# Optimization experiments

Measured on AMD Instinct MI355X. Metric: run time of the kernel, lower is better.

Reference implementation:

```python
import jax, jax.numpy as jnp
import numpy as np
from jax import lax

BS = 8  # block size
NF = 64  # num_feat

def _dct_mat(n=BS):
    k = np.arange(n)
    D = np.cos(np.pi * (2 * k[None, :] + 1) * k[:, None] / (2 * n)) * np.sqrt(2.0 / n)
    D[0] = np.sqrt(1.0 / n)
    return jnp.asarray(D, dtype=jnp.float32)  # orthonormal DCT-II basis [8,8]

D_DCT = _dct_mat()

def conv2d(x, w, b, stride=1, padding=0, dilation=1, groups=1):
    out = lax.conv_general_dilated(
        x, w, window_strides=(stride, stride),
        padding=[(padding, padding), (padding, padding)],
        rhs_dilation=(dilation, dilation),
        feature_group_count=groups,
        dimension_numbers=('NCHW', 'OIHW', 'NCHW'))
    return out + b[None, :, None, None]

def block_dct_idct(x, bs=BS):
    # fused per-8x8-block DDCT followed by IDDCT (orthonormal basis ->
    # mathematically identity, computed explicitly as in the original loop)
    B, C, H, W = x.shape
    xb = x.reshape(B, C, H // bs, bs, W // bs, bs)
    CB = jnp.einsum('ij,bchjwk,lk->bchiwl', D_DCT, xb, D_DCT)   # D X D^T
    out = jnp.einsum('ji,bchjwk,kl->bchiwl', D_DCT, CB, D_DCT)  # D^T Y D
    return out.reshape(B, C, H, W)

def setup_inputs() -> dict:
    key = jax.random.key(0)
    ks = jax.random.split(key, 16)
    s = 0.05
    inp = {
        'x': jax.random.normal(ks[0], (2, 72, 256, 256), dtype=jnp.float32),
        'conv_w': jax.random.normal(ks[1], (64, 72, 3, 3), dtype=jnp.float32) * s,
        'conv_b': jnp.zeros((64,), dtype=jnp.float32),
        # 7 distinct directional_dct_layer instances (branch 6 reuses layer 4's weights, as in the source)
        'ddct_w': jax.random.normal(ks[2], (7, 64, 64, 3, 3), dtype=jnp.float32) * s,
        'ddct_b': jnp.zeros((7, 64), dtype=jnp.float32),
        'dctc_w': jax.random.normal(ks[3], (7, 64, 1, 3, 3), dtype=jnp.float32) * s,  # groups=64 depthwise
        'dctc_b': jnp.zeros((7, 64), dtype=jnp.float32),
        'dw1_w': jax.random.normal(ks[4], (32, 72, 3, 3), dtype=jnp.float32) * s,
        'dw1_b': jnp.zeros((32,), dtype=jnp.float32),
        'dw3_w': jax.random.normal(ks[5], (512, 32, 1, 1), dtype=jnp.float32) * s,
        'dw3_b': jnp.zeros((512,), dtype=jnp.float32),
        'ar_w': jax.random.normal(ks[6], (72, 512, 3, 3), dtype=jnp.float32) * s,
        'ar_b': jnp.zeros((72,), dtype=jnp.float32),
    }
    return inp

def reference(x, conv_w, conv_b, ddct_w, ddct_b, dctc_w, dctc_b,
              dw1_w, dw1_b, dw3_w, dw3_b, ar_w, ar_b):
    B, _, H, W = x.shape
    feat = jax.nn.gelu(conv2d(x, conv_w, conv_b, padding=1), approximate=False)
    # branches use layers [0,1,3,4,5,6(->4),7,8]; branch 6 reuses conv_dct_4
    layer_idx = [0, 1, 2, 3, 4, 3, 5, 6]
    outs = []
    for li in layer_idx:
        y = jax.nn.gelu(conv2d(feat, ddct_w[li], ddct_b[li], padding=1), approximate=False) + feat
        y = conv2d(y, dctc_w[li], dctc_b[li], stride=8, padding=2, dilation=2, groups=NF)
        y = block_dct_idct(y)
        y = jax.image.resize(y, (B, NF, H, W), method='bilinear')  # align_corners=False
        outs.append(y)
    w = jax.nn.sigmoid(conv2d(jax.nn.relu(conv2d(x, dw1_w, dw1_b, padding=1)), dw3_w, dw3_b, padding=0))
    gated = jnp.concatenate([o * w[:, i * NF:(i + 1) * NF] for i, o in enumerate(outs)], axis=1)
    return conv2d(gated, ar_w, ar_b, padding=1)
```

## Files before the change

### kernel.cpp

```cpp
#include <hip/hip_runtime.h>
#include <hip/hip_bf16.h>

#define BB 2
#define HH 256
#define WW 256
#define HW (HH*WW)
#define GP 258
#define GPP (GP*GP)

typedef __attribute__((ext_vector_type(8))) short bf16x8;
typedef __attribute__((ext_vector_type(4))) float f32x4;

__device__ __forceinline__ float geluf(float x) {
    return 0.5f * x * (1.0f + erff(x * 0.7071067811865475f));
}

__device__ __forceinline__ ushort f2bf(float f) {
    __hip_bfloat16 h = __float2bfloat16(f);
    return *reinterpret_cast<ushort*>(&h);
}
__device__ __forceinline__ float bf2f(ushort u) {
    uint v = ((uint)u) << 16;
    return *reinterpret_cast<float*>(&v);
}

__device__ __forceinline__ int dec96(int i) {
    int q = i / 3, r = i - q * 3;
    return q * 8 + (r == 0 ? 0 : (r == 1 ? 2 : 6));
}

__global__ __launch_bounds__(256) void xpose_kernel(
    const float* __restrict__ x, ushort* __restrict__ xt)
{
    const int pix = blockIdx.x * 256 + threadIdx.x;
    const int b   = pix >> 16;
    const int rem = pix & 65535;

    uint w[48];
    const float* xb = x + (size_t)b * 72 * HW + rem;
    #pragma unroll
    for (int i = 0; i < 36; ++i) {
        const ushort lo = f2bf(xb[(size_t)(2 * i)     * HW]);
        const ushort hi = f2bf(xb[(size_t)(2 * i + 1) * HW]);
        w[i] = (uint)lo | ((uint)hi << 16);
    }
    #pragma unroll
    for (int i = 36; i < 48; ++i) w[i] = 0;

    uint* dst = reinterpret_cast<uint*>(xt + (size_t)pix * 96);
    #pragma unroll
    for (int k = 0; k < 12; ++k) {
        uint4 u = { w[4*k], w[4*k+1], w[4*k+2], w[4*k+3] };
        *reinterpret_cast<uint4*>(dst + 4 * k) = u;
    }
}

__global__ __launch_bounds__(256) void prepack_w1_kernel(
    const float* __restrict__ conv_w, const float* __restrict__ dw1_w,
    ushort* __restrict__ wpc1)
{
    const int idx = blockIdx.x * 256 + threadIdx.x;
    if (idx >= 9 * 3 * 6 * 64) return;
    const int lane = idx & 63;
    int rest = idx >> 6;
    const int mf = rest % 6; rest /= 6;
    const int cb = rest % 3;
    const int t  = rest / 3;
    const int co  = mf * 16 + (lane & 15);
    const int ci0 = cb * 32 + (lane >> 4) * 8;
    ushort* dst = wpc1 + (size_t)idx * 8;
    #pragma unroll
    for (int j = 0; j < 8; ++j) {
        const int ci = ci0 + j;
        float w = 0.0f;
        if (ci < 72)
            w = (co < 64) ? conv_w[((size_t)co * 72 + ci) * 9 + t]
                          : dw1_w[((size_t)(co - 64) * 72 + ci) * 9 + t];
        dst[j] = f2bf(w);
    }
}

__global__ __launch_bounds__(256) void conv1dw1_mfma_kernel(
    const ushort* __restrict__ xt, const ushort* __restrict__ wpc1,
    const float* __restrict__ conv_b, const float* __restrict__ dw1_b,
    ushort* __restrict__ fg, float* __restrict__ relu1)
{
    const int lane = threadIdx.x & 63;
    const int wave = threadIdx.x >> 6;
    const int l15  = lane & 15;
    const int lg   = lane >> 4;

    const int bid  = blockIdx.x;
    const int b    = bid >> 9;
    const int rest = bid & 511;
    const int y    = rest >> 1;
    const int x0   = (rest & 1) * 128 + wave * 32;

    f32x4 acc[6][2];
    #pragma unroll
    for (int mf = 0; mf < 6; ++mf)
        #pragma unroll
        for (int nf = 0; nf < 2; ++nf)
            acc[mf][nf] = (f32x4){0.f, 0.f, 0.f, 0.f};

    const bf16x8 zero8 = {};

    #pragma unroll 1
    for (int t = 0; t < 9; ++t) {
        const int dy = t / 3 - 1, dx = t % 3 - 1;
        const int yy = y + dy;
        if ((unsigned)yy >= (unsigned)HH) continue;

        const int xA = x0 + l15 + dx;
        const int xB = xA + 16;
        const bool va = (unsigned)xA < (unsigned)WW;
        const bool vb = (unsigned)xB < (unsigned)WW;
        const int xAc = min(max(xA, 0), WW - 1);
        const int xBc = min(xB, WW - 1);

        const ushort* rowbase = xt + ((size_t)(b * HH + yy) * WW) * 96;
        const ushort* pA = rowbase + (size_t)xAc * 96 + lg * 8;
        const ushort* pB = rowbase + (size_t)xBc * 96 + lg * 8;
        const ushort* wp = wpc1 + (size_t)(t * 3) * (6 * 512) + lane * 8;

        #pragma unroll
        for (int cb = 0; cb < 3; ++cb) {
            bf16x8 B0 = *reinterpret_cast<const bf16x8*>(pA + cb * 32);
            bf16x8 B1 = *reinterpret_cast<const bf16x8*>(pB + cb * 32);
            B0 = va ? B0 : zero8;
            B1 = vb ? B1 : zero8;
            const ushort* wpc = wp + (size_t)cb * (6 * 512);
            #pragma unroll
            for (int mf = 0; mf < 6; ++mf) {
                const bf16x8 A = *reinterpret_cast<const bf16x8*>(wpc + mf * 512);
                acc[mf][0] = __builtin_amdgcn_mfma_f32_16x16x32_bf16(A, B0, acc[mf][0], 0, 0, 0);
                acc[mf][1] = __builtin_amdgcn_mfma_f32_16x16x32_bf16(A, B1, acc[mf][1], 0, 0, 0);
            }
        }
    }

    #pragma unroll
    for (int nf = 0; nf < 2; ++nf) {
        const int xx = x0 + nf * 16 + l15;
        ushort* fgp = fg + ((size_t)(b * HH + y) * WW + xx) * 64;
        #pragma unroll
        for (int mf = 0; mf < 4; ++mf) {
            const int co = mf * 16 + lg * 4;
            ushort pk[4];
            #pragma unroll
            for (int r = 0; r < 4; ++r)
                pk[r] = f2bf(geluf(acc[mf][nf][r] + conv_b[co + r]));
            *reinterpret_cast<uint2*>(fgp + co) = *reinterpret_cast<uint2*>(pk);
        }
    }
    #pragma unroll
    for (int mf = 4; mf < 6; ++mf) {
        const int co = (mf - 4) * 16 + lg * 4;
        #pragma unroll
        for (int nf = 0; nf < 2; ++nf) {
            const int xx = x0 + nf * 16 + l15;
            float* op = relu1 + ((size_t)(b * 32 + co) * HH + y) * WW + xx;
            #pragma unroll
            for (int r = 0; r < 4; ++r)
                op[(size_t)r * HW] = fmaxf(acc[mf][nf][r] + dw1_b[co + r], 0.0f);
        }
    }
}

__global__ __launch_bounds__(256) void prepack_wb_kernel(
    const float* __restrict__ ddct_w, ushort* __restrict__ wpb)
{
    const int idx = blockIdx.x * 256 + threadIdx.x;
    if (idx >= 7 * 9 * 2 * 4 * 64) return;
    const int lane = idx & 63;
    int rest = idx >> 6;
    const int mf = rest & 3; rest >>= 2;
    const int cb = rest & 1; rest >>= 1;
    const int t  = rest % 9;
    const int li = rest / 9;
    const int co  = mf * 16 + (lane & 15);
    const int ci0 = cb * 32 + (lane >> 4) * 8;
    ushort* dst = wpb + (size_t)idx * 8;
    #pragma unroll
    for (int j = 0; j < 8; ++j)
        dst[j] = f2bf(ddct_w[(((size_t)li * 64 + co) * 64 + ci0 + j) * 9 + t]);
}

__global__ __launch_bounds__(256) void branch_mfma_kernel(
    const ushort* __restrict__ fg, const ushort* __restrict__ wpb,
    const float* __restrict__ ddct_b, float* __restrict__ ycomp)
{
    const int lane = threadIdx.x & 63;
    const int wave = threadIdx.x >> 6;
    const int l15  = lane & 15;
    const int lg   = lane >> 4;

    int bid = blockIdx.x;
    const int t72 = bid % 72; bid /= 72;
    const int b  = bid & 1;
    const int li = bid >> 1;
    const int widx = t72 * 4 + wave;
    const int r  = widx / 3;
    const int c0 = (widx - r * 3) * 32;
    const int R  = dec96(r);

    const int cA = c0 + l15, cB = cA + 16;
    const int CA = dec96(cA), CB2 = dec96(cB);

    f32x4 acc[4][2];
    #pragma unroll
    for (int mf = 0; mf < 4; ++mf)
        #pragma unroll
        for (int nf = 0; nf < 2; ++nf)
            acc[mf][nf] = (f32x4){0.f, 0.f, 0.f, 0.f};

    const bf16x8 zero8 = {};
    const ushort* fgb = fg + (size_t)b * HW * 64;

    #pragma unroll 1
    for (int t = 0; t < 9; ++t) {
        const int dy = t / 3 - 1, dx = t % 3 - 1;
        const int yy = R + dy;
        if ((unsigned)yy >= (unsigned)HH) continue;

        const int xA = CA + dx, xB = CB2 + dx;
        const bool va = (unsigned)xA < (unsigned)WW;
        const bool vb = (unsigned)xB < (unsigned)WW;
        const int xAc = min(max(xA, 0), WW - 1);
        const int xBc = min(max(xB, 0), WW - 1);

        const ushort* rowb = fgb + (size_t)yy * WW * 64;
        const ushort* pA = rowb + (size_t)xAc * 64 + lg * 8;
        const ushort* pB = rowb + (size_t)xBc * 64 + lg * 8;
        const ushort* wp = wpb + (size_t)((li * 9 + t) * 2) * (4 * 512) + lane * 8;

        #pragma unroll
        for (int cb = 0; cb < 2; ++cb) {
            bf16x8 B0 = *reinterpret_cast<const bf16x8*>(pA + cb * 32);
            bf16x8 B1 = *reinterpret_cast<const bf16x8*>(pB + cb * 32);
            B0 = va ? B0 : zero8;
            B1 = vb ? B1 : zero8;
            const ushort* wpc = wp + (size_t)cb * (4 * 512);
            #pragma unroll
            for (int mf = 0; mf < 4; ++mf) {
                const bf16x8 A = *reinterpret_cast<const bf16x8*>(wpc + mf * 512);
                acc[mf][0] = __builtin_amdgcn_mfma_f32_16x16x32_bf16(A, B0, acc[mf][0], 0, 0, 0);
                acc[mf][1] = __builtin_amdgcn_mfma_f32_16x16x32_bf16(A, B1, acc[mf][1], 0, 0, 0);
            }
        }
    }

    #pragma unroll
    for (int nf = 0; nf < 2; ++nf) {
        const int c = c0 + nf * 16 + l15;
        const int C = dec96(c);
        const ushort* res = fgb + ((size_t)R * WW + C) * 64;
        #pragma unroll
        for (int mf = 0; mf < 4; ++mf) {
            const int co = mf * 16 + lg * 4;
            ushort r4[4];
            *reinterpret_cast<uint2*>(r4) = *reinterpret_cast<const uint2*>(res + co);
            #pragma unroll
            for (int rr = 0; rr < 4; ++rr) {
                const float v = geluf(acc[mf][nf][rr] + ddct_b[li * 64 + co + rr]) + bf2f(r4[rr]);
                ycomp[((((size_t)li * BB + b) * 64 + co + rr) * 96 + r) * 96 + c] = v;
            }
        }
    }
}

__global__ __launch_bounds__(256) void dctc_kernel(
    const float* __restrict__ ycomp, const float* __restrict__ dctc_w,
    const float* __restrict__ dctc_b, float* __restrict__ s_all)
{
    const int idx = blockIdx.x * 256 + threadIdx.x;
    if (idx >= 7 * BB * 64 * 32 * 32) return;
    const int ow = idx & 31;
    const int oh = (idx >> 5) & 31;
    const int c  = (idx >> 10) & 63;
    const int b  = (idx >> 16) & (BB - 1);
    const int li = idx >> 17;

    const float* yc = ycomp + (((size_t)li * BB + b) * 64 + c) * (96 * 96);
    const float* w  = dctc_w + (li * 64 + c) * 9;
    float acc = dctc_b[li * 64 + c];
    #pragma unroll
    for (int ky = 0; ky < 3; ++ky) {
        const int cr = 3 * oh + ky - 1;
        if (cr < 0) continue;
        #pragma unroll
        for (int kx = 0; kx < 3; ++kx) {
            const int cc = 3 * ow + kx - 1;
            if (cc < 0) continue;
            acc = fmaf(yc[cr * 96 + cc], w[ky * 3 + kx], acc);
        }
    }
    s_all[idx] = acc;
}

__global__ __launch_bounds__(256) void prepack_w3_kernel(
    const float* __restrict__ dw3_w, float* __restrict__ dw3t)
{
    const int idx = blockIdx.x * 256 + threadIdx.x;
    if (idx >= 32 * 512) return;
    const int ch = idx & 511;
    const int k  = idx >> 9;
    dw3t[k * 512 + ch] = dw3_w[ch * 32 + k];
}

__global__ __launch_bounds__(256) void halo_zero_kernel(ushort* __restrict__ gt)
{
    const int PB = 2 * GP * 64 + 2 * 256 * 64;
    const int i = blockIdx.x * 256 + threadIdx.x;
    if (i >= BB * PB) return;
    const int b = i / PB;
    int r = i - b * PB;
    size_t px;
    int c4;
    if (r < 2 * GP * 64) {
        const int rr = r / (GP * 64);
        int rem = r - rr * (GP * 64);
        const int xp = rem / 64; c4 = rem % 64;
        px = (size_t)(rr ? GP - 1 : 0) * GP + xp;
    } else {
        r -= 2 * GP * 64;
        const int side = r / (256 * 64);
        int rem = r - side * (256 * 64);
        const int yp = 1 + rem / 64; c4 = rem % 64;
        px = (size_t)yp * GP + (side ? GP - 1 : 0);
    }
    const uint4 z = {0u, 0u, 0u, 0u};
    *reinterpret_cast<uint4*>(gt + ((size_t)b * GPP + px) * 512 + c4 * 8) = z;
}

__global__ __launch_bounds__(256, 4) void gated_nhwc_kernel(
    const float* __restrict__ relu1, const float* __restrict__ dw3t,
    const float* __restrict__ dw3_b, const float* __restrict__ s_all,
    ushort* __restrict__ gt)
{
    __shared__ float sm[32][16];
    const int pix0 = blockIdx.x * 16;
    const int b  = pix0 >> 16;
    const int y  = (pix0 >> 8) & 255;
    const int x0 = pix0 & 255;

    {
        const int spx = threadIdx.x & 15;
        const int k0  = threadIdx.x >> 4;
        const float* rbase = relu1 + (size_t)b * 32 * HW + (size_t)y * WW + x0 + spx;
        sm[k0][spx]      = rbase[(size_t)k0 * HW];
        sm[k0 + 16][spx] = rbase[(size_t)(k0 + 16) * HW];
    }
    __syncthreads();

    const int ch0 = threadIdx.x * 2;
    const int branch = ch0 >> 6;
    const int c0 = ch0 & 63;
    const int lmap[8] = {0, 1, 2, 3, 4, 3, 5, 6};
    const int li = lmap[branch];

    const float bb0 = dw3_b[ch0], bb1 = dw3_b[ch0 + 1];

    float acc0[16], acc1[16];
    #pragma unroll
    for (int px = 0; px < 16; ++px) { acc0[px] = bb0; acc1[px] = bb1; }

    #pragma unroll
    for (int k = 0; k < 32; ++k) {
        const float2 w2 = *reinterpret_cast<const float2*>(dw3t + k * 512 + ch0);
        const float4* row = reinterpret_cast<const float4*>(&sm[k][0]);
        #pragma unroll
        for (int q = 0; q < 4; ++q) {
            const float4 r4 = row[q];
            acc0[q*4+0] = fmaf(r4.x, w2.x, acc0[q*4+0]);
            acc0[q*4+1] = fmaf(r4.y, w2.x, acc0[q*4+1]);
            acc0[q*4+2] = fmaf(r4.z, w2.x, acc0[q*4+2]);
            acc0[q*4+3] = fmaf(r4.w, w2.x, acc0[q*4+3]);
            acc1[q*4+0] = fmaf(r4.x, w2.y, acc1[q*4+0]);
            acc1[q*4+1] = fmaf(r4.y, w2.y, acc1[q*4+1]);
            acc1[q*4+2] = fmaf(r4.z, w2.y, acc1[q*4+2]);
            acc1[q*4+3] = fmaf(r4.w, w2.y, acc1[q*4+3]);
        }
    }

    const float* sp0 = s_all + (((size_t)li * BB + b) * 64 + c0) * 1024;
    const float* sp1 = sp0 + 1024;

    const float sy = (y + 0.5f) * 0.125f - 0.5f;
    const float fy0f = floorf(sy);
    const float fy = sy - fy0f;
    int y0 = (int)fy0f;
    const int y1 = min(y0 + 1, 31);
    y0 = max(y0, 0);

    float n0[4], n1[4];
    const int xb = (x0 >> 3) - 1;
    #pragma unroll
    for (int jj = 0; jj < 4; ++jj) {
        const int xn = min(max(xb + jj, 0), 31);
        const float a00 = sp0[y0 * 32 + xn], a01 = sp0[y1 * 32 + xn];
        const float a10 = sp1[y0 * 32 + xn], a11 = sp1[y1 * 32 + xn];
        n0[jj] = a00 + fy * (a01 - a00);
        n1[jj] = a10 + fy * (a11 - a10);
    }

    ushort* gbase = gt + (((size_t)b * GPP) + (size_t)(y + 1) * GP + (x0 + 1)) * 512 + ch0;
    #pragma unroll
    for (int px = 0; px < 16; ++px) {
        const int   j  = (px + 4) >> 3;
        const float fx = (float)((px + 4) & 7) * 0.125f + 0.0625f;
        const float va = n0[j] + fx * (n0[j + 1] - n0[j]);
        const float vb = n1[j] + fx * (n1[j + 1] - n1[j]);
        const float g0 = 1.0f / (1.0f + exp2f(-1.4426950408889634f * acc0[px]));
        const float g1 = 1.0f / (1.0f + exp2f(-1.4426950408889634f * acc1[px]));
        const uint pack = (uint)f2bf(va * g0) | ((uint)f2bf(vb * g1) << 16);
        *reinterpret_cast<uint*>(gbase + (size_t)px * 512) = pack;
    }
}

__global__ __launch_bounds__(256) void prepack_w_kernel(
    const float* __restrict__ ar_w, ushort* __restrict__ wpack)
{
    const int idx = blockIdx.x * 256 + threadIdx.x;
    if (idx >= 16 * 9 * 5 * 64) return;
    const int lane = idx & 63;
    int rest = idx >> 6;
    const int mf = rest % 5; rest /= 5;
    const int t  = rest % 9;
    const int cb = rest / 9;
    const int co  = mf * 16 + (lane & 15);
    const int ci0 = cb * 32 + (lane >> 4) * 8;
    ushort* dst = wpack + (size_t)idx * 8;
    #pragma unroll
    for (int j = 0; j < 8; ++j) {
        const float w = (co < 72) ? ar_w[((size_t)co * 512 + ci0 + j) * 9 + t] : 0.0f;
        dst[j] = f2bf(w);
    }
}

#define WPK_CHUNK (9 * 5 * 512)

__global__ __launch_bounds__(256, 2) void conv_ar_mfma_kernel(
    const ushort* __restrict__ gt, const ushort* __restrict__ wpack,
    const float* __restrict__ ar_b, float* __restrict__ out)
{
    __shared__ ushort smw[WPK_CHUNK];
    const int tid  = threadIdx.x;
    const int lane = tid & 63;
    const int wave = tid >> 6;
    const int l15  = lane & 15;
    const int lg   = lane >> 4;

    const int lb = (blockIdx.x & 7) * 64 + (blockIdx.x >> 3);
    const int b  = lb >> 8;
    const int y  = lb & 255;
    const int x0 = wave * 64;

    f32x4 acc[5][4];
    #pragma unroll
    for (int mf = 0; mf < 5; ++mf)
        #pragma unroll
        for (int nf = 0; nf < 4; ++nf)
            acc[mf][nf] = (f32x4){0.f, 0.f, 0.f, 0.f};

    const ushort* rowp[3];
    #pragma unroll
    for (int dy = 0; dy < 3; ++dy)
        rowp[dy] = gt + ((size_t)b * GPP + (size_t)(y + dy) * GP) * 512;
    int off[3][4];
    #pragma unroll
    for (int dx = 0; dx < 3; ++dx)
        #pragma unroll
        for (int nf = 0; nf < 4; ++nf)
            off[dx][nf] = (x0 + nf * 16 + l15 + dx) * 512 + lg * 8;

    uint4 streg[12];
    {
        const uint4* s = reinterpret_cast<const uint4*>(wpack);
        #pragma unroll
        for (int i = 0; i < 12; ++i) {
            const int e = i * 256 + tid;
            streg[i] = (e < 2880) ? s[e] : (uint4){0u, 0u, 0u, 0u};
        }
        uint4* d = reinterpret_cast<uint4*>(smw);
        #pragma unroll
        for (int i = 0; i < 12; ++i) {
            const int e = i * 256 + tid;
            if (e < 2880) d[e] = streg[i];
        }
    }
    __syncthreads();

    #pragma unroll 1
    for (int cb = 0; cb < 16; ++cb) {
        if (cb < 15) {
            const uint4* s = reinterpret_cast<const uint4*>(
                wpack + (size_t)(cb + 1) * WPK_CHUNK);
            #pragma unroll
            for (int i = 0; i < 12; ++i) {
                const int e = i * 256 + tid;
                if (e < 2880) streg[i] = s[e];
            }
        }

        const int cbo = cb * 32;
        bf16x8 Bcur[4], Bnxt[4];
        #pragma unroll
        for (int nf = 0; nf < 4; ++nf)
            Bcur[nf] = *reinterpret_cast<const bf16x8*>(rowp[0] + off[0][nf] + cbo);

        #pragma unroll
        for (int t = 0; t < 9; ++t) {
            if (t < 8) {
                const int dyn = (t + 1) / 3, dxn = (t + 1) % 3;
                #pragma unroll
                for (int nf = 0; nf < 4; ++nf)
                    Bnxt[nf] = *reinterpret_cast<const bf16x8*>(
                        rowp[dyn] + off[dxn][nf] + cbo);
            }
            __builtin_amdgcn_s_setprio(1);
            #pragma unroll
            for (int mf = 0; mf < 5; ++mf) {
                const bf16x8 A = *reinterpret_cast<const bf16x8*>(
                    smw + (t * 5 + mf) * 512 + lane * 8);
                #pragma unroll
                for (int nf = 0; nf < 4; ++nf)
                    acc[mf][nf] = __builtin_amdgcn_mfma_f32_16x16x32_bf16(
                        A, Bcur[nf], acc[mf][nf], 0, 0, 0);
            }
            __builtin_amdgcn_s_setprio(0);
            if (t < 8) {
                #pragma unroll
                for (int nf = 0; nf < 4; ++nf) Bcur[nf] = Bnxt[nf];
            }
        }

        __syncthreads();
        if (cb < 15) {
            uint4* d = reinterpret_cast<uint4*>(smw);
            #pragma unroll
            for (int i = 0; i < 12; ++i) {
                const int e = i * 256 + tid;
                if (e < 2880) d[e] = streg[i];
            }
        }
        __syncthreads();
    }

    #pragma unroll
    for (int mf = 0; mf < 5; ++mf) {
        const int co = mf * 16 + lg * 4;
        if (co >= 72) continue;
        #pragma unroll
        for (int nf = 0; nf < 4; ++nf) {
            const int x = x0 + nf * 16 + l15;
            float* op = out + (((size_t)(b * 72 + co) * HH + y) * WW) + x;
            #pragma unroll
            for (int r = 0; r < 4; ++r)
                op[(size_t)r * HW] = acc[mf][nf][r] + ar_b[co + r];
        }
    }
}

extern "C" void kernel_launch(void* const* d_in, const int* in_sizes, int n_in,
                              void* d_out, int out_size, void* d_ws, size_t ws_size,
                              hipStream_t stream) {
    const float* x      = (const float*)d_in[0];
    const float* conv_w = (const float*)d_in[1];
    const float* conv_b = (const float*)d_in[2];
    const float* ddct_w = (const float*)d_in[3];
    const float* ddct_b = (const float*)d_in[4];
    const float* dctc_w = (const float*)d_in[5];
    const float* dctc_b = (const float*)d_in[6];
    const float* dw1_w  = (const float*)d_in[7];
    const float* dw1_b  = (const float*)d_in[8];
    const float* dw3_w  = (const float*)d_in[9];
    const float* dw3_b  = (const float*)d_in[10];
    const float* ar_w   = (const float*)d_in[11];
    const float* ar_b   = (const float*)d_in[12];
    float* out = (float*)d_out;

    float* ws = (float*)d_ws;
    ushort* gated_t = (ushort*)ws;
    ushort* fg    = (ushort*)ws;
    float* ycomp  = ws + 4194304;
    float* s_all  = ws + 34080768;
    float* relu1  = ws + 34998272;
    ushort* wpack = (ushort*)(ws + 39192576);
    ushort* wpb   = (ushort*)(ws + 39376896);
    ushort* wpc1  = (ushort*)(ws + 39505920);
    ushort* xt    = (ushort*)(ws + 39547392);
    float* dw3t   = ws + 45838848;

    prepack_w_kernel<<<dim3(180), dim3(256), 0, stream>>>(ar_w, wpack);
    prepack_wb_kernel<<<dim3(126), dim3(256), 0, stream>>>(ddct_w, wpb);
    prepack_w1_kernel<<<dim3(41), dim3(256), 0, stream>>>(conv_w, dw1_w, wpc1);
    prepack_w3_kernel<<<dim3(64), dim3(256), 0, stream>>>(dw3_w, dw3t);
    xpose_kernel<<<dim3(BB * HW / 256), dim3(256), 0, stream>>>(x, xt);

    conv1dw1_mfma_kernel<<<dim3(BB * HH * 2), dim3(256), 0, stream>>>(
        xt, wpc1, conv_b, dw1_b, fg, relu1);

    branch_mfma_kernel<<<dim3(7 * BB * 72), dim3(256), 0, stream>>>(
        fg, wpb, ddct_b, ycomp);

    dctc_kernel<<<dim3((7 * BB * 64 * 32 * 32) / 256), dim3(256), 0, stream>>>(
        ycomp, dctc_w, dctc_b, s_all);

    halo_zero_kernel<<<dim3(514), dim3(256), 0, stream>>>(gated_t);

    gated_nhwc_kernel<<<dim3(BB * HW / 16), dim3(256), 0, stream>>>(
        relu1, dw3t, dw3_b, s_all, gated_t);

    conv_ar_mfma_kernel<<<dim3(BB * HH), dim3(256), 0, stream>>>(
        gated_t, wpack, ar_b, out);
}
```

Measured before the change: 414.8 us.

## Compute 1x1 gate conv with MFMA and store relu1 as NHWC bf16

Replaces the scalar FMA gated kernel with one that runs the 32->512 1x1 conv on bf16 MFMA instructions. The relu1 intermediate is now written channel-last in bf16 rather than planar fp32, and the dw3 weights are prepacked into the MFMA fragment layout. Bilinear row interpolation nodes are precomputed into shared memory once per 64-pixel block. This cuts intermediate traffic and ALU work in the gate stage, at the cost of bf16 rounding of the relu and gate weights.

```diff
diff --git a/kernel.cpp b/kernel.cpp
--- a/kernel.cpp
+++ b/kernel.cpp
@@ -83,7 +83,7 @@
 __global__ __launch_bounds__(256) void conv1dw1_mfma_kernel(
     const ushort* __restrict__ xt, const ushort* __restrict__ wpc1,
     const float* __restrict__ conv_b, const float* __restrict__ dw1_b,
-    ushort* __restrict__ fg, float* __restrict__ relu1)
+    ushort* __restrict__ fg, ushort* __restrict__ relu1t)
 {
     const int lane = threadIdx.x & 63;
     const int wave = threadIdx.x >> 6;
@@ -159,10 +159,12 @@
         #pragma unroll
         for (int nf = 0; nf < 2; ++nf) {
             const int xx = x0 + nf * 16 + l15;
-            float* op = relu1 + ((size_t)(b * 32 + co) * HH + y) * WW + xx;
+            ushort pk[4];
             #pragma unroll
             for (int r = 0; r < 4; ++r)
-                op[(size_t)r * HW] = fmaxf(acc[mf][nf][r] + dw1_b[co + r], 0.0f);
+                pk[r] = f2bf(fmaxf(acc[mf][nf][r] + dw1_b[co + r], 0.0f));
+            *reinterpret_cast<uint2*>(relu1t + ((size_t)(b * HH + y) * WW + xx) * 32 + co) =
+                *reinterpret_cast<uint2*>(pk);
         }
     }
 }
@@ -298,14 +300,19 @@
     s_all[idx] = acc;
 }
 
-__global__ __launch_bounds__(256) void prepack_w3_kernel(
-    const float* __restrict__ dw3_w, float* __restrict__ dw3t)
+__global__ __launch_bounds__(256) void prepack_wg_kernel(
+    const float* __restrict__ dw3_w, ushort* __restrict__ wg)
 {
     const int idx = blockIdx.x * 256 + threadIdx.x;
-    if (idx >= 32 * 512) return;
-    const int ch = idx & 511;
-    const int k  = idx >> 9;
-    dw3t[k * 512 + ch] = dw3_w[ch * 32 + k];
+    if (idx >= 2048) return;
+    const int lane = idx & 63;
+    const int ct = idx >> 6;
+    const int ch = ct * 16 + (lane & 15);
+    const int k0 = (lane >> 4) * 8;
+    ushort* dst = wg + (size_t)idx * 8;
+    #pragma unroll
+    for (int j = 0; j < 8; ++j)
+        dst[j] = f2bf(dw3_w[(size_t)ch * 32 + k0 + j]);
 }
 
 __global__ __launch_bounds__(256) void halo_zero_kernel(ushort* __restrict__ gt)
@@ -333,58 +340,22 @@
     *reinterpret_cast<uint4*>(gt + ((size_t)b * GPP + px) * 512 + c4 * 8) = z;
 }
 
-__global__ __launch_bounds__(256, 4) void gated_nhwc_kernel(
-    const float* __restrict__ relu1, const float* __restrict__ dw3t,
+__global__ __launch_bounds__(256, 2) void gated_mfma_kernel(
+    const ushort* __restrict__ relu1t, const ushort* __restrict__ wg,
     const float* __restrict__ dw3_b, const float* __restrict__ s_all,
     ushort* __restrict__ gt)
 {
-    __shared__ float sm[32][16];
-    const int pix0 = blockIdx.x * 16;
-    const int b  = pix0 >> 16;
-    const int y  = (pix0 >> 8) & 255;
-    const int x0 = pix0 & 255;
-
-    {
-        const int spx = threadIdx.x & 15;
-        const int k0  = threadIdx.x >> 4;
-        const float* rbase = relu1 + (size_t)b * 32 * HW + (size_t)y * WW + x0 + spx;
-        sm[k0][spx]      = rbase[(size_t)k0 * HW];
-        sm[k0 + 16][spx] = rbase[(size_t)(k0 + 16) * HW];
-    }
-    __syncthreads();
-
-    const int ch0 = threadIdx.x * 2;
-    const int branch = ch0 >> 6;
-    const int c0 = ch0 & 63;
-    const int lmap[8] = {0, 1, 2, 3, 4, 3, 5, 6};
-    const int li = lmap[branch];
-
-    const float bb0 = dw3_b[ch0], bb1 = dw3_b[ch0 + 1];
-
-    float acc0[16], acc1[16];
-    #pragma unroll
-    for (int px = 0; px < 16; ++px) { acc0[px] = bb0; acc1[px] = bb1; }
-
-    #pragma unroll
-    for (int k = 0; k < 32; ++k) {
-        const float2 w2 = *reinterpret_cast<const float2*>(dw3t + k * 512 + ch0);
-        const float4* row = reinterpret_cast<const float4*>(&sm[k][0]);
-        #pragma unroll
-        for (int q = 0; q < 4; ++q) {
-            const float4 r4 = row[q];
-            acc0[q*4+0] = fmaf(r4.x, w2.x, acc0[q*4+0]);
-            acc0[q*4+1] = fmaf(r4.y, w2.x, acc0[q*4+1]);
-            acc0[q*4+2] = fmaf(r4.z, w2.x, acc0[q*4+2]);
-            acc0[q*4+3] = fmaf(r4.w, w2.x, acc0[q*4+3]);
-            acc1[q*4+0] = fmaf(r4.x, w2.y, acc1[q*4+0]);
-            acc1[q*4+1] = fmaf(r4.y, w2.y, acc1[q*4+1]);
-            acc1[q*4+2] = fmaf(r4.z, w2.y, acc1[q*4+2]);
-            acc1[q*4+3] = fmaf(r4.w, w2.y, acc1[q*4+3]);
-        }
-    }
-
-    const float* sp0 = s_all + (((size_t)li * BB + b) * 64 + c0) * 1024;
-    const float* sp1 = sp0 + 1024;
+    __shared__ float nodes[5120];
+    const int tid  = threadIdx.x;
+    const int lane = tid & 63;
+    const int wave = tid >> 6;
+    const int l15  = lane & 15;
+    const int lg   = lane >> 4;
+
+    const int bid = blockIdx.x;
+    const int b  = bid >> 10;
+    const int y  = (bid >> 2) & 255;
+    const int x0 = (bid & 3) * 64;
 
     const float sy = (y + 0.5f) * 0.125f - 0.5f;
     const float fy0f = floorf(sy);
@@ -392,29 +363,57 @@
     int y0 = (int)fy0f;
     const int y1 = min(y0 + 1, 31);
     y0 = max(y0, 0);
-
-    float n0[4], n1[4];
     const int xb = (x0 >> 3) - 1;
-    #pragma unroll
-    for (int jj = 0; jj < 4; ++jj) {
-        const int xn = min(max(xb + jj, 0), 31);
-        const float a00 = sp0[y0 * 32 + xn], a01 = sp0[y1 * 32 + xn];
-        const float a10 = sp1[y0 * 32 + xn], a11 = sp1[y1 * 32 + xn];
-        n0[jj] = a00 + fy * (a01 - a00);
-        n1[jj] = a10 + fy * (a11 - a10);
-    }
-
-    ushort* gbase = gt + (((size_t)b * GPP) + (size_t)(y + 1) * GP + (x0 + 1)) * 512 + ch0;
-    #pragma unroll
-    for (int px = 0; px < 16; ++px) {
-        const int   j  = (px + 4) >> 3;
-        const float fx = (float)((px + 4) & 7) * 0.125f + 0.0625f;
-        const float va = n0[j] + fx * (n0[j + 1] - n0[j]);
-        const float vb = n1[j] + fx * (n1[j + 1] - n1[j]);
-        const float g0 = 1.0f / (1.0f + exp2f(-1.4426950408889634f * acc0[px]));
-        const float g1 = 1.0f / (1.0f + exp2f(-1.4426950408889634f * acc1[px]));
-        const uint pack = (uint)f2bf(va * g0) | ((uint)f2bf(vb * g1) << 16);
-        *reinterpret_cast<uint*>(gbase + (size_t)px * 512) = pack;
+
+    const int lmap[8] = {0, 1, 2, 3, 4, 3, 5, 6};
+    #pragma unroll 1
+    for (int e = tid; e < 5120; e += 256) {
+        const int ch = e / 10, j = e - ch * 10;
+        const int li = lmap[ch >> 6];
+        const float* sp = s_all + (((size_t)li * BB + b) * 64 + (ch & 63)) * 1024;
+        const int xn = min(max(xb + j, 0), 31);
+        const float a0 = sp[y0 * 32 + xn], a1 = sp[y1 * 32 + xn];
+        nodes[e] = a0 + fy * (a1 - a0);
+    }
+    __syncthreads();
+
+    bf16x8 Bv[4];
+    const ushort* rb = relu1t + ((size_t)(b * HH + y) * WW + x0) * 32;
+    #pragma unroll
+    for (int pxt = 0; pxt < 4; ++pxt)
+        Bv[pxt] = *reinterpret_cast<const bf16x8*>(rb + (pxt * 16 + l15) * 32 + lg * 8);
+
+    ushort* gy = gt + (((size_t)b * GPP) + (size_t)(y + 1) * GP + (x0 + 1)) * 512;
+    const f32x4 zero4 = {0.f, 0.f, 0.f, 0.f};
+
+    #pragma unroll 1
+    for (int i = 0; i < 8; ++i) {
+        const int ct = wave * 8 + i;
+        const bf16x8 A = *reinterpret_cast<const bf16x8*>(wg + (size_t)(ct * 64 + lane) * 8);
+        const int ch0 = ct * 16 + lg * 4;
+        const float4 bb = *reinterpret_cast<const float4*>(dw3_b + ch0);
+        const float bias4[4] = {bb.x, bb.y, bb.z, bb.w};
+        f32x4 acc[4];
+        #pragma unroll
+        for (int pxt = 0; pxt < 4; ++pxt)
+            acc[pxt] = __builtin_amdgcn_mfma_f32_16x16x32_bf16(A, Bv[pxt], zero4, 0, 0, 0);
+        #pragma unroll
+        for (int pxt = 0; pxt < 4; ++pxt) {
+            const int pxl = pxt * 16 + l15;
+            const int jl = (pxl + 4) >> 3;
+            const float fx = (float)((pxl + 4) & 7) * 0.125f + 0.0625f;
+            ushort pk[4];
+            #pragma unroll
+            for (int r = 0; r < 4; ++r) {
+                const int ch = ch0 + r;
+                const float g = 1.0f / (1.0f + exp2f(-1.4426950408889634f * (acc[pxt][r] + bias4[r])));
+                const float n0v = nodes[ch * 10 + jl];
+                const float n1v = nodes[ch * 10 + jl + 1];
+                const float v = n0v + fx * (n1v - n0v);
+                pk[r] = f2bf(v * g);
+            }
+            *reinterpret_cast<uint2*>(gy + (size_t)pxl * 512 + ch0) = *reinterpret_cast<uint2*>(pk);
+        }
     }
 }
 
@@ -585,21 +584,21 @@
     ushort* fg    = (ushort*)ws;
     float* ycomp  = ws + 4194304;
     float* s_all  = ws + 34080768;
-    float* relu1  = ws + 34998272;
+    ushort* relu1t = (ushort*)(ws + 34998272);
     ushort* wpack = (ushort*)(ws + 39192576);
     ushort* wpb   = (ushort*)(ws + 39376896);
     ushort* wpc1  = (ushort*)(ws + 39505920);
     ushort* xt    = (ushort*)(ws + 39547392);
-    float* dw3t   = ws + 45838848;
+    ushort* wg    = (ushort*)(ws + 45838848);
 
     prepack_w_kernel<<<dim3(180), dim3(256), 0, stream>>>(ar_w, wpack);
     prepack_wb_kernel<<<dim3(126), dim3(256), 0, stream>>>(ddct_w, wpb);
     prepack_w1_kernel<<<dim3(41), dim3(256), 0, stream>>>(conv_w, dw1_w, wpc1);
-    prepack_w3_kernel<<<dim3(64), dim3(256), 0, stream>>>(dw3_w, dw3t);
+    prepack_wg_kernel<<<dim3(8), dim3(256), 0, stream>>>(dw3_w, wg);
     xpose_kernel<<<dim3(BB * HW / 256), dim3(256), 0, stream>>>(x, xt);
 
     conv1dw1_mfma_kernel<<<dim3(BB * HH * 2), dim3(256), 0, stream>>>(
-        xt, wpc1, conv_b, dw1_b, fg, relu1);
+        xt, wpc1, conv_b, dw1_b, fg, relu1t);
 
     branch_mfma_kernel<<<dim3(7 * BB * 72), dim3(256), 0, stream>>>(
         fg, wpb, ddct_b, ycomp);
@@ -609,8 +608,8 @@
 
     halo_zero_kernel<<<dim3(514), dim3(256), 0, stream>>>(gated_t);
 
-    gated_nhwc_kernel<<<dim3(BB * HW / 16), dim3(256), 0, stream>>>(
-        relu1, dw3t, dw3_b, s_all, gated_t);
+    gated_mfma_kernel<<<dim3(BB * HH * 4), dim3(256), 0, stream>>>(
+        relu1t, wg, dw3_b, s_all, gated_t);
 
     conv_ar_mfma_kernel<<<dim3(BB * HH), dim3(256), 0, stream>>>(
         gated_t, wpack, ar_b, out);
```

Result: faster. 339.1 us, median of 2 (-18.3%).
